# Kernel tuning notes

Measured on AMD Instinct MI355X. Metric: run time of the kernel, lower is better.

## Reference

```python
import jax, jax.numpy as jnp
import numpy as np

N = 50000
E = 800000
H = 256
ED = 13
EPS = 1e-5


def silu(x):
    return x * jax.nn.sigmoid(x)


def layernorm(x, g, b):
    mu = jnp.mean(x, axis=-1, keepdims=True)
    var = jnp.var(x, axis=-1, keepdims=True)
    return (x - mu) * jax.lax.rsqrt(var + EPS) * g + b


def setup_inputs() -> dict:
    key = jax.random.key(0)
    ks = jax.random.split(key, 24)
    s = 0.02
    d = {
        "h": jax.random.normal(ks[0], (N, H), jnp.float32),
        "pos": jax.random.normal(ks[1], (N, 3), jnp.float32),
        "edge_index": jax.random.randint(ks[2], (2, E), 0, N, jnp.int32),
        "edge_attr": jax.random.normal(ks[3], (E, ED), jnp.float32),
        # edge_mlp: Linear(2H+1+ED -> 2H), SiLU, LN(2H), Linear(2H -> H), SiLU
        "W_e1": jax.random.normal(ks[4], (2 * H + 1 + ED, 2 * H), jnp.float32) * s,
        "b_e1": jnp.zeros((2 * H,), jnp.float32),
        "g_e": jnp.ones((2 * H,), jnp.float32),
        "be_ln": jnp.zeros((2 * H,), jnp.float32),
        "W_e2": jax.random.normal(ks[5], (2 * H, H), jnp.float32) * s,
        "b_e2": jnp.zeros((H,), jnp.float32),
        # node_mlp: Linear(2H -> 2H), SiLU, LN(2H), Linear(2H -> H)
        "W_n1": jax.random.normal(ks[6], (2 * H, 2 * H), jnp.float32) * s,
        "b_n1": jnp.zeros((2 * H,), jnp.float32),
        "g_n": jnp.ones((2 * H,), jnp.float32),
        "bn_ln": jnp.zeros((2 * H,), jnp.float32),
        "W_n2": jax.random.normal(ks[7], (2 * H, H), jnp.float32) * s,
        "b_n2": jnp.zeros((H,), jnp.float32),
        # outer LayerNorm(H)
        "g_o": jnp.ones((H,), jnp.float32),
        "bo_ln": jnp.zeros((H,), jnp.float32),
        # coord_mlp: Linear(H->H), SiLU, Linear(H->1, no bias, weight*0.001)
        "W_c1": jax.random.normal(ks[8], (H, H), jnp.float32) * s,
        "b_c1": jnp.zeros((H,), jnp.float32),
        "W_c2": jax.random.normal(ks[9], (H, 1), jnp.float32) * 0.001,
        # att_mlp: Linear(H->1), Sigmoid
        "W_a": jax.random.normal(ks[10], (H, 1), jnp.float32) * s,
        "b_a": jnp.zeros((1,), jnp.float32),
        # coord_feedback: Linear(1->H), SiLU, Linear(H->H)
        "W_f1": jax.random.normal(ks[11], (1, H), jnp.float32) * s,
        "b_f1": jnp.zeros((H,), jnp.float32),
        "W_f2": jax.random.normal(ks[12], (H, H), jnp.float32) * s,
        "b_f2": jnp.zeros((H,), jnp.float32),
    }
    return d


def reference(h, pos, edge_index, edge_attr,
              W_e1, b_e1, g_e, be_ln, W_e2, b_e2,
              W_n1, b_n1, g_n, bn_ln, W_n2, b_n2,
              g_o, bo_ln,
              W_c1, b_c1, W_c2,
              W_a, b_a,
              W_f1, b_f1, W_f2, b_f2):
    row, col = edge_index[0], edge_index[1]
    diff = pos[row] - pos[col]                                  # [E,3]
    dist = jnp.maximum(jnp.linalg.norm(diff, axis=-1, keepdims=True), 1e-5)
    edge_in = jnp.concatenate([h[row], h[col], dist, edge_attr], axis=-1)
    m = silu(layernorm(silu(edge_in @ W_e1 + b_e1), g_e, be_ln) @ W_e2 + b_e2)  # [E,H]
    att = jax.nn.sigmoid(m @ W_a + b_a)                         # [E,1]
    agg = jax.ops.segment_sum(m * att, row, num_segments=N)     # [N,H]
    node_in = jnp.concatenate([h, agg], axis=-1)
    h_upd = layernorm(silu(node_in @ W_n1 + b_n1), g_n, bn_ln) @ W_n2 + b_n2
    h_new = layernorm(h + h_upd, g_o, bo_ln)
    coord_w = silu(m @ W_c1 + b_c1) @ W_c2                      # [E,1]
    coord_agg = jax.ops.segment_sum(diff * coord_w, row, num_segments=N)
    pos_new = pos + coord_agg
    diff_new = pos_new[row] - pos_new[col]
    dist_new = jnp.maximum(jnp.linalg.norm(diff_new, axis=-1, keepdims=True), 1e-5)
    coord_fb = silu(dist_new @ W_f1 + b_f1) @ W_f2 + b_f2       # [E,H]
    fb_agg = jax.ops.segment_sum(coord_fb, row, num_segments=N)
    h_new = h_new + 0.1 * fb_agg
    return (h_new, pos_new)
```

## Files before the change

kernel.cpp:

```cpp
#include <hip/hip_runtime.h>


#define NN 50000
#define EE 800000

typedef unsigned short u16;
typedef float f32x4 __attribute__((ext_vector_type(4)));
typedef short bf16x8 __attribute__((ext_vector_type(8)));
typedef unsigned uint4v __attribute__((ext_vector_type(4)));

__device__ __forceinline__ u16 f2bf(float f) {
  unsigned u = __float_as_uint(f);
  u = (u + 0x7FFFu + ((u >> 16) & 1u)) >> 16;
  return (u16)u;
}
__device__ __forceinline__ float bf2f(u16 s) {
  return __uint_as_float(((unsigned)s) << 16);
}
__device__ __forceinline__ float bflo(unsigned u) { return __uint_as_float(u << 16); }
__device__ __forceinline__ float bfhi(unsigned u) { return __uint_as_float(u & 0xFFFF0000u); }
__device__ __forceinline__ float silu_f(float x) {
  return x * __builtin_amdgcn_rcpf(1.f + exp2f(x * -1.44269504f));
}

__device__ __forceinline__ void gload16(const void* g, void* l) {
  __builtin_amdgcn_global_load_lds(
      (const __attribute__((address_space(1))) void*)g,
      (__attribute__((address_space(3))) void*)l, 16, 0, 0);
}

__global__ __launch_bounds__(256, 2) void edge_fused(
    const u16* __restrict__ P1, const u16* __restrict__ P2,
    const float* __restrict__ dist, const float* __restrict__ eattr,
    const float* __restrict__ Wt, const float* __restrict__ ge,
    const float* __restrict__ beln, const float* __restrict__ be2,
    const float* __restrict__ bc1, const float* __restrict__ Wa,
    const float* __restrict__ ba, const float* __restrict__ Wc2,
    const u16* __restrict__ We2f, const u16* __restrict__ Wc1f,
    const int* __restrict__ rowp, const int* __restrict__ colp,
    const int* __restrict__ perm, const int* __restrict__ meta, int cidx,
    u16* __restrict__ mBuf, float* __restrict__ att, float* __restrict__ cwv) {
  const int M = meta[2 * cidx + 1];
  const int eb = meta[2 * cidx];
  const int m0 = blockIdx.x * 64;
  if (m0 >= M) return;
  __shared__ __align__(16) u16 At[64][512];
  const int tid = threadIdx.x, w = tid >> 6, lane = tid & 63;
  const int l15 = lane & 15, kq = lane >> 4;
  const int ch0 = lane * 8;

  {
    int le0 = m0 + w * 16 + (lane & 15);
    if (le0 > M - 1) le0 = M - 1;
    const int e_l = perm[eb + le0];
    const int r_l = rowp[e_l];
    const int c_l = colp[e_l];
    const float dd_l = dist[e_l];

    float wreg[8][15], gg[8], bb[8];
#pragma unroll
    for (int i = 0; i < 8; i++) {
#pragma unroll
      for (int j = 0; j < 15; j++) wreg[i][j] = Wt[(ch0 + i) * 16 + j];
      gg[i] = ge[ch0 + i]; bb[i] = beln[ch0 + i];
    }
#pragma unroll 2
    for (int rr = 0; rr < 16; rr++) {
      int e = __shfl(e_l, rr);
      int r = __shfl(r_l, rr);
      int c = __shfl(c_l, rr);
      float dd = __shfl(dd_l, rr);
      float fa[13];
#pragma unroll
      for (int j = 0; j < 13; j++) fa[j] = eattr[(size_t)e * 13 + j];
      uint4v u1 = *(const uint4v*)&P1[(size_t)r * 512 + ch0];
      uint4v u2 = *(const uint4v*)&P2[(size_t)c * 512 + ch0];
      float sv[8], s1 = 0.f, s2 = 0.f;
#pragma unroll
      for (int i = 0; i < 8; i++) {
        float xp = (i & 1) ? bfhi(u1[i >> 1]) : bflo(u1[i >> 1]);
        float xq = (i & 1) ? bfhi(u2[i >> 1]) : bflo(u2[i >> 1]);
        float x = xp + xq + wreg[i][0] + dd * wreg[i][1];
#pragma unroll
        for (int j = 0; j < 13; j++) x = fmaf(fa[j], wreg[i][2 + j], x);
        float s = silu_f(x);
        sv[i] = s; s1 += s; s2 += s * s;
      }
#pragma unroll
      for (int o = 32; o; o >>= 1) { s1 += __shfl_xor(s1, o); s2 += __shfl_xor(s2, o); }
      float mu = s1 * (1.f / 512.f);
      float inv = rsqrtf(s2 * (1.f / 512.f) - mu * mu + 1e-5f);
      int row = w * 16 + rr;
      u16 ot[8];
#pragma unroll
      for (int i = 0; i < 8; i++) ot[i] = f2bf((sv[i] - mu) * inv * gg[i] + bb[i]);
      *(uint4v*)&At[row][(lane ^ (row & 7)) * 8] = *(const uint4v*)ot;
    }
  }
  __syncthreads();

  f32x4 acc[4][4] = {};
  {
    const u16* Bw = We2f + (size_t)w * 32768;
    __builtin_amdgcn_s_setprio(1);
#pragma unroll 4
    for (int ks = 0; ks < 16; ks++) {
      bf16x8 bfr[4], af[4];
#pragma unroll
      for (int j = 0; j < 4; j++)
        bfr[j] = *(const bf16x8*)&Bw[((ks * 4 + j) * 64 + lane) * 8];
#pragma unroll
      for (int i = 0; i < 4; i++) {
        int rw = i * 16 + l15;
        af[i] = *(const bf16x8*)&At[rw][((ks * 4 + kq) ^ (rw & 7)) * 8];
      }
#pragma unroll
      for (int i = 0; i < 4; i++)
#pragma unroll
        for (int j = 0; j < 4; j++)
          acc[i][j] = __builtin_amdgcn_mfma_f32_16x16x32_bf16(af[i], bfr[j], acc[i][j], 0, 0, 0);
    }
    __builtin_amdgcn_s_setprio(0);
  }
  __syncthreads();

  u16* Mt = &At[0][0];
  float* red = (float*)&At[32][0];
  float ds_a[4][4];
#pragma unroll
  for (int i = 0; i < 4; i++)
#pragma unroll
    for (int t = 0; t < 4; t++) ds_a[i][t] = 0.f;
#pragma unroll
  for (int j = 0; j < 4; j++) {
    int col = w * 64 + j * 16 + l15;
    float bz = be2[col], wa = Wa[col];
    int slot = col >> 3, offc = col & 7;
#pragma unroll
    for (int i = 0; i < 4; i++) {
#pragma unroll
      for (int t = 0; t < 4; t++) {
        int row = i * 16 + kq * 4 + t;
        float sv = silu_f(acc[i][j][t] + bz);
        int le = m0 + row;
        if (le < M) mBuf[(size_t)le * 256 + col] = f2bf(sv);
        Mt[row * 256 + ((slot ^ (row & 7)) << 3) + offc] = f2bf(sv);
        ds_a[i][t] += sv * wa;
      }
    }
  }
#pragma unroll
  for (int i = 0; i < 4; i++)
#pragma unroll
    for (int t = 0; t < 4; t++) {
      float s = ds_a[i][t];
      s += __shfl_xor(s, 1); s += __shfl_xor(s, 2);
      s += __shfl_xor(s, 4); s += __shfl_xor(s, 8);
      if (l15 == 0) red[(i * 16 + kq * 4 + t) * 4 + w] = s;
    }
  __syncthreads();
  if (tid < 64) {
    int le = m0 + tid;
    if (le < M) {
      float s = red[tid * 4] + red[tid * 4 + 1] + red[tid * 4 + 2] + red[tid * 4 + 3] + ba[0];
      att[le] = __builtin_amdgcn_rcpf(1.f + exp2f(s * -1.44269504f));
    }
  }

  f32x4 ac2[4][4] = {};
  {
    const u16* Bw = Wc1f + (size_t)w * 16384;
    __builtin_amdgcn_s_setprio(1);
#pragma unroll 4
    for (int ks = 0; ks < 8; ks++) {
      bf16x8 bfr[4], af[4];
#pragma unroll
      for (int j = 0; j < 4; j++)
        bfr[j] = *(const bf16x8*)&Bw[((ks * 4 + j) * 64 + lane) * 8];
#pragma unroll
      for (int i = 0; i < 4; i++) {
        int rw = i * 16 + l15;
        af[i] = *(const bf16x8*)&Mt[rw * 256 + (((ks * 4 + kq) ^ (rw & 7)) << 3)];
      }
#pragma unroll
      for (int i = 0; i < 4; i++)
#pragma unroll
        for (int j = 0; j < 4; j++)
          ac2[i][j] = __builtin_amdgcn_mfma_f32_16x16x32_bf16(af[i], bfr[j], ac2[i][j], 0, 0, 0);
    }
    __builtin_amdgcn_s_setprio(0);
  }
  float ds_c[4][4];
#pragma unroll
  for (int i = 0; i < 4; i++)
#pragma unroll
    for (int t = 0; t < 4; t++) ds_c[i][t] = 0.f;
#pragma unroll
  for (int j = 0; j < 4; j++) {
    int col = w * 64 + j * 16 + l15;
    float bz = bc1[col], wc = Wc2[col];
#pragma unroll
    for (int i = 0; i < 4; i++)
#pragma unroll
      for (int t = 0; t < 4; t++)
        ds_c[i][t] += silu_f(ac2[i][j][t] + bz) * wc;
  }
  __syncthreads();
#pragma unroll
  for (int i = 0; i < 4; i++)
#pragma unroll
    for (int t = 0; t < 4; t++) {
      float s = ds_c[i][t];
      s += __shfl_xor(s, 1); s += __shfl_xor(s, 2);
      s += __shfl_xor(s, 4); s += __shfl_xor(s, 8);
      if (l15 == 0) red[(i * 16 + kq * 4 + t) * 4 + w] = s;
    }
  __syncthreads();
  if (tid < 64) {
    int le = m0 + tid;
    if (le < M)
      cwv[le] = red[tid * 4] + red[tid * 4 + 1] + red[tid * 4 + 2] + red[tid * 4 + 3];
  }
}

template <int MODE, int GATHER>
__global__ __launch_bounds__(256) void gemm128(
    const u16* __restrict__ A, const u16* __restrict__ BT,
    const float* __restrict__ bias, void* __restrict__ outp,
    int Mh, int Nc, int K,
    const u16* __restrict__ hbf, const u16* __restrict__ src2,
    const float* __restrict__ cnt, const float* __restrict__ b2, float scale) {
  const int M = Mh;
  const int m0 = blockIdx.x * 128, n0 = blockIdx.y * 128;
  if (m0 >= M) return;
  __shared__ __align__(16) u16 As[128][32];
  __shared__ __align__(16) u16 Bs[128][32];
  const int tid = threadIdx.x, w = tid >> 6, lane = tid & 63;
  const int srow = lane >> 2, sch = (lane & 3) * 8;
  const int r0 = w * 32 + srow, r1 = r0 + 16;

  u16* as0 = &As[w * 32][0];
  u16* as1 = &As[w * 32 + 16][0];
  u16* bs0 = &Bs[w * 32][0];
  u16* bs1 = &Bs[w * 32 + 16][0];

  const u16 *a0r, *a0c, *a1r, *a1c;
  a0c = a1c = nullptr;
  if (GATHER == 2) {
    int q0 = m0 + r0; if (q0 > M - 1) q0 = M - 1;
    int q1 = m0 + r1; if (q1 > M - 1) q1 = M - 1;
    a0r = hbf + (size_t)q0 * 256;  a0c = src2 + (size_t)q0 * 256;
    a1r = hbf + (size_t)q1 * 256;  a1c = src2 + (size_t)q1 * 256;
  } else {
    a0r = A + (size_t)(m0 + r0) * K;
    a1r = A + (size_t)(m0 + r1) * K;
  }
  const u16* b0 = BT + (size_t)(n0 + r0) * K;
  const u16* b1 = BT + (size_t)(n0 + r1) * K;

  f32x4 acc[4][4] = {};
  const int l15 = lane & 15, ko = (lane >> 4) * 8;
  const int ar0 = (w >> 1) * 64, br0 = (w & 1) * 64;

  for (int k0 = 0; k0 < K; k0 += 32) {
    const u16 *pa0, *pa1;
    if (GATHER == 2) {
      if (k0 < 256) { pa0 = a0r + k0;         pa1 = a1r + k0; }
      else          { pa0 = a0c + (k0 - 256); pa1 = a1c + (k0 - 256); }
    } else { pa0 = a0r + k0; pa1 = a1r + k0; }
    gload16(pa0 + sch, as0);
    gload16(pa1 + sch, as1);
    gload16(b0 + k0 + sch, bs0);
    gload16(b1 + k0 + sch, bs1);
    __syncthreads();
    bf16x8 af[4], bfr[4];
#pragma unroll
    for (int i = 0; i < 4; i++)
      af[i] = *reinterpret_cast<const bf16x8*>(&As[ar0 + i * 16 + l15][ko]);
#pragma unroll
    for (int j = 0; j < 4; j++)
      bfr[j] = *reinterpret_cast<const bf16x8*>(&Bs[br0 + j * 16 + l15][ko]);
#pragma unroll
    for (int i = 0; i < 4; i++)
#pragma unroll
      for (int j = 0; j < 4; j++)
        acc[i][j] = __builtin_amdgcn_mfma_f32_16x16x32_bf16(af[i], bfr[j], acc[i][j], 0, 0, 0);
    __syncthreads();
  }

  const int rb = m0 + ar0 + ((lane >> 4) << 2);
#pragma unroll
  for (int j = 0; j < 4; j++) {
    const int gc = n0 + br0 + j * 16 + l15;
    const float bz = (MODE == 2 || MODE == 7) ? 0.f : bias[gc];
#pragma unroll
    for (int i = 0; i < 4; i++) {
#pragma unroll
      for (int t = 0; t < 4; t++) {
        const int gr = rb + i * 16 + t;
        if (gr >= M) continue;
        float v = acc[i][j][t] + bz;
        size_t oi = (size_t)gr * Nc + gc;
        if (MODE == 0)      ((u16*)outp)[oi] = f2bf(silu_f(v));
        else if (MODE == 1) ((float*)outp)[oi] = v;
        else if (MODE == 2) ((float*)outp)[oi] += scale * (v + cnt[gr] * b2[gc]);
        else if (MODE == 7) ((u16*)outp)[oi] = f2bf(v);
      }
    }
  }
}

__global__ void wtrans(const float* __restrict__ src, u16* __restrict__ dst,
                       int K, int Nn, int Kpad) {
  int t = blockIdx.x * 256 + threadIdx.x;
  if (t >= Nn * Kpad) return;
  int n = t / Kpad, k = t - n * Kpad;
  float v = (k < K) ? src[(size_t)k * Nn + n] : 0.f;
  dst[t] = f2bf(v);
}

__global__ void build_wf(const float* __restrict__ src, u16* __restrict__ dst,
                         int K, int Nn) {
  int t = blockIdx.x * 256 + threadIdx.x;
  if (t >= Nn * K) return;
  int i = t & 7;
  int lane = (t >> 3) & 63;
  int rest = t >> 9;
  int j = rest & 3;
  int rest2 = rest >> 2;
  int KS = K >> 5;
  int wv = rest2 / KS, ks = rest2 - wv * KS;
  int n = wv * 64 + j * 16 + (lane & 15);
  int k = ks * 32 + (lane >> 4) * 8 + i;
  dst[t] = f2bf(src[(size_t)k * Nn + n]);
}

__global__ void build_wt(const float* __restrict__ W_e1, const float* __restrict__ b_e1,
                         float* __restrict__ Wt) {
  int t = blockIdx.x * 256 + threadIdx.x;
  if (t >= 512 * 16) return;
  int n = t >> 4, j = t & 15;
  float v = 0.f;
  if (j == 0) v = b_e1[n];
  else if (j < 15) v = W_e1[(size_t)(511 + j) * 512 + n];
  Wt[t] = v;
}

__global__ void edge_geom(const float* __restrict__ pos, const int* __restrict__ row,
                          const int* __restrict__ colx, float* __restrict__ dist,
                          int* __restrict__ icnt) {
  int e = blockIdx.x * 256 + threadIdx.x;
  if (e >= EE) return;
  int r = row[e], c = colx[e];
  float d0 = pos[r * 3 + 0] - pos[c * 3 + 0];
  float d1 = pos[r * 3 + 1] - pos[c * 3 + 1];
  float d2 = pos[r * 3 + 2] - pos[c * 3 + 2];
  dist[e] = fmaxf(sqrtf(d0 * d0 + d1 * d1 + d2 * d2), 1e-5f);
  atomicAdd(&icnt[r], 1);
}

__global__ __launch_bounds__(1024) void scan_ptr(const int* __restrict__ icnt,
                                                 int* __restrict__ ptr) {
  __shared__ int ls[1024];
  const int t = threadIdx.x;
  const int SEG = (NN + 1023) / 1024;
  int s0 = t * SEG;
  int s1 = s0 + SEG; if (s1 > NN) s1 = NN;
  int sum = 0;
  for (int i = s0; i < s1; i++) sum += icnt[i];
  ls[t] = sum;
  __syncthreads();
  for (int off = 1; off < 1024; off <<= 1) {
    int v = (t >= off) ? ls[t - off] : 0;
    __syncthreads();
    ls[t] += v;
    __syncthreads();
  }
  int run = ls[t] - sum;
  for (int i = s0; i < s1; i++) { ptr[i] = run; run += icnt[i]; }
  if (t == 1023) ptr[NN] = ls[1023];
}

__global__ void copy_head(const int* __restrict__ ptr, int* __restrict__ head,
                          float* __restrict__ cntf) {
  int n = blockIdx.x * 256 + threadIdx.x;
  if (n >= NN) return;
  head[n] = ptr[n];
  cntf[n] = (float)(ptr[n + 1] - ptr[n]);
}

__global__ void fill_perm(const int* __restrict__ row, int* __restrict__ head,
                          int* __restrict__ perm) {
  int e = blockIdx.x * 256 + threadIdx.x;
  if (e >= EE) return;
  int p = atomicAdd(&head[row[e]], 1);
  perm[p] = e;
}

__global__ void chunk_meta(const int* __restrict__ ptr, int* __restrict__ meta,
                           int CN, int nch, int capE) {
  int c = blockIdx.x * 256 + threadIdx.x;
  if (c >= nch) return;
  int lo = c * CN;
  int hi = lo + CN; if (hi > NN) hi = NN;
  int b = ptr[lo];
  int cc = ptr[hi] - b;
  if (cc > capE) cc = capE;
  meta[2 * c + 0] = b;
  meta[2 * c + 1] = cc;
}

__global__ __launch_bounds__(128) void ln_512(u16* __restrict__ t,
                                              const float* __restrict__ g,
                                              const float* __restrict__ b, int Mh) {
  int row = blockIdx.x;
  if (row >= Mh) return;
  int tid = threadIdx.x;
  size_t base = (size_t)row * 512 + tid * 4;
  ushort4 xv = *reinterpret_cast<const ushort4*>(&t[base]);
  float x0 = bf2f(xv.x), x1 = bf2f(xv.y), x2 = bf2f(xv.z), x3 = bf2f(xv.w);
  float s1 = x0 + x1 + x2 + x3;
  float s2 = x0 * x0 + x1 * x1 + x2 * x2 + x3 * x3;
  for (int o = 32; o; o >>= 1) { s1 += __shfl_xor(s1, o); s2 += __shfl_xor(s2, o); }
  __shared__ float red[4];
  if ((tid & 63) == 0) { red[tid >> 6] = s1; red[2 + (tid >> 6)] = s2; }
  __syncthreads();
  s1 = red[0] + red[1]; s2 = red[2] + red[3];
  float mu = s1 * (1.f / 512.f);
  float var = s2 * (1.f / 512.f) - mu * mu;
  float inv = rsqrtf(var + 1e-5f);
  int c = tid * 4;
  ushort4 yv;
  yv.x = f2bf((x0 - mu) * inv * g[c + 0] + b[c + 0]);
  yv.y = f2bf((x1 - mu) * inv * g[c + 1] + b[c + 1]);
  yv.z = f2bf((x2 - mu) * inv * g[c + 2] + b[c + 2]);
  yv.w = f2bf((x3 - mu) * inv * g[c + 3] + b[c + 3]);
  *reinterpret_cast<ushort4*>(&t[base]) = yv;
}

__global__ __launch_bounds__(256) void node_agg(
    const u16* __restrict__ m, const float* __restrict__ att,
    const float* __restrict__ cwv,
    const float* __restrict__ pos, const int* __restrict__ colx,
    const int* __restrict__ perm, const int* __restrict__ ptr,
    const int* __restrict__ meta, int cidx,
    u16* __restrict__ aggbf, float* __restrict__ cagg, int nlo, int cn) {
  int w = threadIdx.x >> 6, lane = threadIdx.x & 63;
  int nl = blockIdx.x * 4 + w;
  if (nl >= cn) return;
  int n = nlo + nl;
  int base = meta[2 * cidx];
  int p0 = ptr[n], p1 = ptr[n + 1];
  const int half = lane >> 5, ch = (lane & 31) * 8;
  float a[8] = {};
  for (int p = p0 + half; p < p1; p += 2) {
    int le = p - base;
    float at = att[le];
    uint4v mv = *reinterpret_cast<const uint4v*>(&m[(size_t)le * 256 + ch]);
#pragma unroll
    for (int i = 0; i < 4; i++) {
      a[2 * i]     += at * bflo(mv[i]);
      a[2 * i + 1] += at * bfhi(mv[i]);
    }
  }
#pragma unroll
  for (int i = 0; i < 8; i++) a[i] += __shfl_xor(a[i], 32);
  if (half == 0) {
    u16 ot[8];
#pragma unroll
    for (int i = 0; i < 8; i++) ot[i] = f2bf(a[i]);
    *reinterpret_cast<uint4v*>(&aggbf[(size_t)n * 256 + ch]) =
        *reinterpret_cast<const uint4v*>(ot);
  }
  float prx = pos[n * 3 + 0], pry = pos[n * 3 + 1], prz = pos[n * 3 + 2];
  float sx = 0.f, sy = 0.f, sz = 0.f;
  for (int p = p0 + lane; p < p1; p += 64) {
    int le = p - base;
    float cv = cwv[le];
    int c = colx[perm[p]];
    sx += cv * (prx - pos[c * 3 + 0]);
    sy += cv * (pry - pos[c * 3 + 1]);
    sz += cv * (prz - pos[c * 3 + 2]);
  }
#pragma unroll
  for (int o = 32; o; o >>= 1) {
    sx += __shfl_xor(sx, o); sy += __shfl_xor(sy, o); sz += __shfl_xor(sz, o);
  }
  if (lane == 0) {
    cagg[n * 3 + 0] = sx; cagg[n * 3 + 1] = sy; cagg[n * 3 + 2] = sz;
  }
}

__global__ __launch_bounds__(64) void hmid_ln(const float* __restrict__ h,
                                              const float* __restrict__ hupd,
                                              const float* __restrict__ g,
                                              const float* __restrict__ b,
                                              float* __restrict__ outp) {
  int row = blockIdx.x, lane = threadIdx.x;
  size_t base = (size_t)row * 256 + lane * 4;
  float x[4];
#pragma unroll
  for (int i = 0; i < 4; i++) x[i] = h[base + i] + hupd[base + i];
  float s1 = x[0] + x[1] + x[2] + x[3];
  float s2 = x[0] * x[0] + x[1] * x[1] + x[2] * x[2] + x[3] * x[3];
  for (int o = 32; o; o >>= 1) { s1 += __shfl_xor(s1, o); s2 += __shfl_xor(s2, o); }
  float mu = s1 * (1.f / 256.f);
  float var = s2 * (1.f / 256.f) - mu * mu;
  float inv = rsqrtf(var + 1e-5f);
#pragma unroll
  for (int i = 0; i < 4; i++)
    outp[base + i] = (x[i] - mu) * inv * g[lane * 4 + i] + b[lane * 4 + i];
}

__global__ void posnew_k(const float* __restrict__ pos, const float* __restrict__ cagg,
                         float* __restrict__ op) {
  int t = blockIdx.x * 256 + threadIdx.x;
  if (t >= NN * 3) return;
  op[t] = pos[t] + cagg[t];
}

__global__ void dnn_k(const float* __restrict__ posn, const int* __restrict__ rowp,
                      const int* __restrict__ colp, const int* __restrict__ perm,
                      float* __restrict__ dnc) {
  int p = blockIdx.x * 256 + threadIdx.x;
  if (p >= EE) return;
  int e = perm[p];
  int r = rowp[e], c = colp[e];
  float d0 = posn[r * 3 + 0] - posn[c * 3 + 0];
  float d1 = posn[r * 3 + 1] - posn[c * 3 + 1];
  float d2 = posn[r * 3 + 2] - posn[c * 3 + 2];
  dnc[p] = fmaxf(sqrtf(d0 * d0 + d1 * d1 + d2 * d2), 1e-5f);
}

__global__ __launch_bounds__(256) void edge_fb2(
    const float* __restrict__ dnc, const int* __restrict__ ptr,
    const float* __restrict__ Wf1, const float* __restrict__ bf1,
    u16* __restrict__ Sbf) {
  int w = threadIdx.x >> 6, lane = threadIdx.x & 63;
  int n = blockIdx.x * 4 + w;
  if (n >= NN) return;
  const float L2E = 1.44269504f;
  float w0 = Wf1[lane * 4 + 0], w1 = Wf1[lane * 4 + 1];
  float w2 = Wf1[lane * 4 + 2], w3 = Wf1[lane * 4 + 3];
  float b0 = bf1[lane * 4 + 0], b1 = bf1[lane * 4 + 1];
  float b2 = bf1[lane * 4 + 2], b3 = bf1[lane * 4 + 3];
  float wl0 = -w0 * L2E, wl1 = -w1 * L2E, wl2 = -w2 * L2E, wl3 = -w3 * L2E;
  float bl0 = -b0 * L2E, bl1 = -b1 * L2E, bl2 = -b2 * L2E, bl3 = -b3 * L2E;
  float a0 = 0.f, a1 = 0.f, a2 = 0.f, a3 = 0.f;
  int p0 = ptr[n], p1 = ptr[n + 1];
  for (int p = p0; p < p1; p++) {
    float dn = dnc[p];
    float x0 = fmaf(dn, w0, b0), e0 = exp2f(fmaf(dn, wl0, bl0));
    float x1 = fmaf(dn, w1, b1), e1 = exp2f(fmaf(dn, wl1, bl1));
    float x2 = fmaf(dn, w2, b2), e2 = exp2f(fmaf(dn, wl2, bl2));
    float x3 = fmaf(dn, w3, b3), e3 = exp2f(fmaf(dn, wl3, bl3));
    a0 += x0 * __builtin_amdgcn_rcpf(1.f + e0);
    a1 += x1 * __builtin_amdgcn_rcpf(1.f + e1);
    a2 += x2 * __builtin_amdgcn_rcpf(1.f + e2);
    a3 += x3 * __builtin_amdgcn_rcpf(1.f + e3);
  }
  ushort4 ov;
  ov.x = f2bf(a0); ov.y = f2bf(a1); ov.z = f2bf(a2); ov.w = f2bf(a3);
  *reinterpret_cast<ushort4*>(&Sbf[(size_t)n * 256 + lane * 4]) = ov;
}

__global__ void cvt_bf(const float* __restrict__ src, u16* __restrict__ dst, int n) {
  int t = blockIdx.x * 256 + threadIdx.x;
  if (t < n) dst[t] = f2bf(src[t]);
}

extern "C" void kernel_launch(void* const* d_in, const int* in_sizes, int n_in,
                              void* d_out, int out_size, void* d_ws, size_t ws_size,
                              hipStream_t stream) {
  const float* h     = (const float*)d_in[0];
  const float* pos   = (const float*)d_in[1];
  const int*   eidx  = (const int*)d_in[2];
  const float* eattr = (const float*)d_in[3];
  const float* W_e1 = (const float*)d_in[4];  const float* b_e1 = (const float*)d_in[5];
  const float* g_e  = (const float*)d_in[6];  const float* be_ln = (const float*)d_in[7];
  const float* W_e2 = (const float*)d_in[8];  const float* b_e2 = (const float*)d_in[9];
  const float* W_n1 = (const float*)d_in[10]; const float* b_n1 = (const float*)d_in[11];
  const float* g_n  = (const float*)d_in[12]; const float* bn_ln = (const float*)d_in[13];
  const float* W_n2 = (const float*)d_in[14]; const float* b_n2 = (const float*)d_in[15];
  const float* g_o  = (const float*)d_in[16]; const float* bo_ln = (const float*)d_in[17];
  const float* W_c1 = (const float*)d_in[18]; const float* b_c1 = (const float*)d_in[19];
  const float* W_c2 = (const float*)d_in[20];
  const float* W_a  = (const float*)d_in[21]; const float* b_a = (const float*)d_in[22];
  const float* W_f1 = (const float*)d_in[23]; const float* b_f1 = (const float*)d_in[24];
  const float* W_f2 = (const float*)d_in[25]; const float* b_f2 = (const float*)d_in[26];

  float* outp = (float*)d_out;
  float* out_pos = outp + (size_t)NN * 256;

  char* base = (char*)d_ws;
  size_t off = 0;
  auto alloc = [&](size_t bytes) -> void* {
    off = (off + 255) & ~(size_t)255;
    void* p = base + off;
    off += bytes;
    return p;
  };
  const int NP = 50048;
  u16* We1Ta = (u16*)alloc((size_t)512 * 256 * 2);
  u16* We1Tb = (u16*)alloc((size_t)512 * 256 * 2);
  u16* We2f  = (u16*)alloc((size_t)256 * 512 * 2);
  u16* Wc1f  = (u16*)alloc((size_t)256 * 256 * 2);
  u16* Wn1T  = (u16*)alloc((size_t)512 * 512 * 2);
  u16* Wn2T  = (u16*)alloc((size_t)256 * 512 * 2);
  u16* Wf2T  = (u16*)alloc((size_t)256 * 256 * 2);
  float* Wt  = (float*)alloc((size_t)512 * 16 * 4);
  u16* hbf   = (u16*)alloc((size_t)NP * 256 * 2);
  float* dist = (float*)alloc((size_t)EE * 4);
  int*   icnt = (int*)alloc((size_t)NN * 4);
  int*   ptr  = (int*)alloc((size_t)(NN + 1) * 4);
  int*   head = (int*)alloc((size_t)NN * 4);
  int*   perm = (int*)alloc((size_t)EE * 4);
  float* cntf = (float*)alloc((size_t)NN * 4);
  float* cagg = (float*)alloc((size_t)NN * 12);
  int*   meta = (int*)alloc((size_t)8192);
  u16*   aggbf = (u16*)alloc((size_t)NP * 256 * 2);
  u16*   P1 = (u16*)alloc((size_t)NP * 512 * 2);
  u16*   P2 = (u16*)alloc((size_t)NP * 512 * 2);

  off = (off + 255) & ~(size_t)255;
  char* arena = base + off;
  size_t avail = (ws_size > off) ? ws_size - off : 0;
  const size_t SBF_BYTES = (size_t)NP * 256 * 2;
  const int ladder[6] = {16384, 12288, 8192, 4096, 2048, 1024};
  int CN = 1024;
  for (int li = 0; li < 6; li++) {
    size_t need = (size_t)((size_t)ladder[li] * 16 + 4096) * 520;
    if (need < SBF_BYTES) need = SBF_BYTES;
    if (need <= avail) { CN = ladder[li]; break; }
  }
  const int capE = CN * 16 + 4096;
  u16*   mBuf = (u16*)arena;
  float* att  = (float*)(arena + (size_t)capE * 512);
  float* cw   = (float*)(arena + (size_t)capE * 516);
  u16*   Sbf  = (u16*)arena;
  u16*   t2   = P1;
  float* hupd = (float*)P2;

  const int* rowp = eidx;
  const int* colp = eidx + EE;
  const int nch = (NN + CN - 1) / CN;

  hipMemsetAsync(icnt, 0, (size_t)NN * 4, stream);

  wtrans<<<(512 * 256 + 255) / 256, 256, 0, stream>>>(W_e1, We1Ta, 256, 512, 256);
  wtrans<<<(512 * 256 + 255) / 256, 256, 0, stream>>>(W_e1 + (size_t)256 * 512, We1Tb, 256, 512, 256);
  build_wf<<<(256 * 512 + 255) / 256, 256, 0, stream>>>(W_e2, We2f, 512, 256);
  build_wf<<<(256 * 256 + 255) / 256, 256, 0, stream>>>(W_c1, Wc1f, 256, 256);
  wtrans<<<(512 * 512 + 255) / 256, 256, 0, stream>>>(W_n1, Wn1T, 512, 512, 512);
  wtrans<<<(256 * 512 + 255) / 256, 256, 0, stream>>>(W_n2, Wn2T, 512, 256, 512);
  wtrans<<<(256 * 256 + 255) / 256, 256, 0, stream>>>(W_f2, Wf2T, 256, 256, 256);
  build_wt<<<(512 * 16 + 255) / 256, 256, 0, stream>>>(W_e1, b_e1, Wt);
  cvt_bf<<<(NN * 256 + 255) / 256, 256, 0, stream>>>(h, hbf, NN * 256);

  edge_geom<<<(EE + 255) / 256, 256, 0, stream>>>(pos, rowp, colp, dist, icnt);
  scan_ptr<<<1, 1024, 0, stream>>>(icnt, ptr);
  copy_head<<<(NN + 255) / 256, 256, 0, stream>>>(ptr, head, cntf);
  fill_perm<<<(EE + 255) / 256, 256, 0, stream>>>(rowp, head, perm);
  chunk_meta<<<(nch + 255) / 256, 256, 0, stream>>>(ptr, meta, CN, nch, capE);

  dim3 gp(NP / 128, 4);
  gemm128<7, 0><<<gp, 256, 0, stream>>>(hbf, We1Ta, nullptr, P1, NN, 512, 256,
                                        nullptr, nullptr, nullptr, nullptr, 0.f);
  gemm128<7, 0><<<gp, 256, 0, stream>>>(hbf, We1Tb, nullptr, P2, NN, 512, 256,
                                        nullptr, nullptr, nullptr, nullptr, 0.f);

  for (int c = 0; c < nch; c++) {
    int nlo = c * CN;
    int cn = NN - nlo; if (cn > CN) cn = CN;
    edge_fused<<<capE / 64, 256, 0, stream>>>(
        P1, P2, dist, eattr, Wt, g_e, be_ln, b_e2, b_c1, W_a, b_a, W_c2,
        We2f, Wc1f, rowp, colp, perm, meta, c, mBuf, att, cw);
    node_agg<<<(cn + 3) / 4, 256, 0, stream>>>(mBuf, att, cw, pos, colp, perm, ptr,
                                               meta, c, aggbf, cagg, nlo, cn);
  }

  gemm128<0, 2><<<gp, 256, 0, stream>>>(nullptr, Wn1T, b_n1, t2, NN, 512, 512,
                                        hbf, aggbf, nullptr, nullptr, 0.f);
  ln_512<<<NN, 128, 0, stream>>>(t2, g_n, bn_ln, NN);
  dim3 g5(NP / 128, 2);
  gemm128<1, 0><<<g5, 256, 0, stream>>>(t2, Wn2T, b_n2, hupd, NN, 256, 512,
                                        nullptr, nullptr, nullptr, nullptr, 0.f);
  hmid_ln<<<NN, 64, 0, stream>>>(h, hupd, g_o, bo_ln, outp);

  posnew_k<<<(NN * 3 + 255) / 256, 256, 0, stream>>>(pos, cagg, out_pos);
  dnn_k<<<(EE + 255) / 256, 256, 0, stream>>>(out_pos, rowp, colp, perm, dist);
  edge_fb2<<<(NN + 3) / 4, 256, 0, stream>>>(dist, ptr, W_f1, b_f1, Sbf);
  gemm128<2, 0><<<g5, 256, 0, stream>>>(Sbf, Wf2T, nullptr, outp, NN, 256, 256,
                                        nullptr, nullptr, cntf, b_f2, 0.1f);
}
```

Baseline: 1.941 ms.

## Compute first edge-MLP layer per edge with MFMA instead of node-level projections

Replaces the precomputed node-level projections P1/P2 (h@W_e1 halves, gathered per edge) with a per-edge MFMA GEMM over the full 527-wide edge input. The kernel gathers h rows by row/col index and reads a per-chunk bf16 tail buffer holding bias, distance and edge attributes, built by a new small kernel. The LayerNorm reduction now goes through shared memory across waves. This trades two node GEMMs and their 512-wide gathers for about 16x more first-layer FLOPs on edges. It also enlarges the chunk-size ladder and adds a kernel launch per chunk.

```diff
diff --git a/kernel.cpp b/kernel.cpp
--- a/kernel.cpp
+++ b/kernel.cpp
@@ -30,13 +30,13 @@
 }
 
 __global__ __launch_bounds__(256, 2) void edge_fused(
-    const u16* __restrict__ P1, const u16* __restrict__ P2,
-    const float* __restrict__ dist, const float* __restrict__ eattr,
-    const float* __restrict__ Wt, const float* __restrict__ ge,
-    const float* __restrict__ beln, const float* __restrict__ be2,
-    const float* __restrict__ bc1, const float* __restrict__ Wa,
-    const float* __restrict__ ba, const float* __restrict__ Wc2,
-    const u16* __restrict__ We2f, const u16* __restrict__ Wc1f,
+    const u16* __restrict__ hbf, const u16* __restrict__ tail,
+    const float* __restrict__ ge, const float* __restrict__ beln,
+    const float* __restrict__ be2, const float* __restrict__ bc1,
+    const float* __restrict__ Wa, const float* __restrict__ ba,
+    const float* __restrict__ Wc2,
+    const u16* __restrict__ We1f, const u16* __restrict__ We2f,
+    const u16* __restrict__ Wc1f,
     const int* __restrict__ rowp, const int* __restrict__ colp,
     const int* __restrict__ perm, const int* __restrict__ meta, int cidx,
     u16* __restrict__ mBuf, float* __restrict__ att, float* __restrict__ cwv) {
@@ -47,55 +47,106 @@
   __shared__ __align__(16) u16 At[64][512];
   const int tid = threadIdx.x, w = tid >> 6, lane = tid & 63;
   const int l15 = lane & 15, kq = lane >> 4;
-  const int ch0 = lane * 8;
-
+
+  int ridx[4], cidx4[4], tle[4];
+#pragma unroll
+  for (int i = 0; i < 4; i++) {
+    int le = m0 + i * 16 + l15; if (le > M - 1) le = M - 1;
+    tle[i] = le;
+    int e = perm[eb + le];
+    ridx[i] = rowp[e]; cidx4[i] = colp[e];
+  }
+  float gg[8], bb[8];
+#pragma unroll
+  for (int j = 0; j < 8; j++) {
+    int col = w * 128 + j * 16 + l15;
+    gg[j] = ge[col]; bb[j] = beln[col];
+  }
+
+  f32x4 acc1[4][8] = {};
   {
-    int le0 = m0 + w * 16 + (lane & 15);
-    if (le0 > M - 1) le0 = M - 1;
-    const int e_l = perm[eb + le0];
-    const int r_l = rowp[e_l];
-    const int c_l = colp[e_l];
-    const float dd_l = dist[e_l];
-
-    float wreg[8][15], gg[8], bb[8];
-#pragma unroll
-    for (int i = 0; i < 8; i++) {
-#pragma unroll
-      for (int j = 0; j < 15; j++) wreg[i][j] = Wt[(ch0 + i) * 16 + j];
-      gg[i] = ge[ch0 + i]; bb[i] = beln[ch0 + i];
-    }
-#pragma unroll 2
-    for (int rr = 0; rr < 16; rr++) {
-      int e = __shfl(e_l, rr);
-      int r = __shfl(r_l, rr);
-      int c = __shfl(c_l, rr);
-      float dd = __shfl(dd_l, rr);
-      float fa[13];
-#pragma unroll
-      for (int j = 0; j < 13; j++) fa[j] = eattr[(size_t)e * 13 + j];
-      uint4v u1 = *(const uint4v*)&P1[(size_t)r * 512 + ch0];
-      uint4v u2 = *(const uint4v*)&P2[(size_t)c * 512 + ch0];
-      float sv[8], s1 = 0.f, s2 = 0.f;
-#pragma unroll
-      for (int i = 0; i < 8; i++) {
-        float xp = (i & 1) ? bfhi(u1[i >> 1]) : bflo(u1[i >> 1]);
-        float xq = (i & 1) ? bfhi(u2[i >> 1]) : bflo(u2[i >> 1]);
-        float x = xp + xq + wreg[i][0] + dd * wreg[i][1];
-#pragma unroll
-        for (int j = 0; j < 13; j++) x = fmaf(fa[j], wreg[i][2 + j], x);
-        float s = silu_f(x);
-        sv[i] = s; s1 += s; s2 += s * s;
-      }
-#pragma unroll
-      for (int o = 32; o; o >>= 1) { s1 += __shfl_xor(s1, o); s2 += __shfl_xor(s2, o); }
-      float mu = s1 * (1.f / 512.f);
-      float inv = rsqrtf(s2 * (1.f / 512.f) - mu * mu + 1e-5f);
-      int row = w * 16 + rr;
-      u16 ot[8];
-#pragma unroll
-      for (int i = 0; i < 8; i++) ot[i] = f2bf((sv[i] - mu) * inv * gg[i] + bb[i]);
-      *(uint4v*)&At[row][(lane ^ (row & 7)) * 8] = *(const uint4v*)ot;
-    }
+    const u16* Bw1 = We1f + (size_t)w * 69632;
+    for (int ks = 0; ks < 17; ks++) {
+      bf16x8 af[4];
+#pragma unroll
+      for (int i = 0; i < 4; i++) {
+        const u16* ap;
+        if (ks < 8)       ap = hbf + (size_t)ridx[i] * 256 + ks * 32 + kq * 8;
+        else if (ks < 16) ap = hbf + (size_t)cidx4[i] * 256 + (ks - 8) * 32 + kq * 8;
+        else              ap = tail + (size_t)tle[i] * 32 + kq * 8;
+        af[i] = *(const bf16x8*)ap;
+      }
+      __builtin_amdgcn_s_setprio(1);
+#pragma unroll
+      for (int j = 0; j < 8; j++) {
+        bf16x8 bfr = *(const bf16x8*)&Bw1[((size_t)(ks * 8 + j) * 64 + lane) * 8];
+#pragma unroll
+        for (int i = 0; i < 4; i++)
+          acc1[i][j] = __builtin_amdgcn_mfma_f32_16x16x32_bf16(af[i], bfr, acc1[i][j], 0, 0, 0);
+      }
+      __builtin_amdgcn_s_setprio(0);
+    }
+  }
+
+  {
+    float* red2 = (float*)&At[0][0];
+    float s1a[4][4], s2a[4][4];
+#pragma unroll
+    for (int i = 0; i < 4; i++)
+#pragma unroll
+      for (int t = 0; t < 4; t++) { s1a[i][t] = 0.f; s2a[i][t] = 0.f; }
+#pragma unroll
+    for (int i = 0; i < 4; i++)
+#pragma unroll
+      for (int j = 0; j < 8; j++)
+#pragma unroll
+        for (int t = 0; t < 4; t++) {
+          float sv = silu_f(acc1[i][j][t]);
+          acc1[i][j][t] = sv;
+          s1a[i][t] += sv; s2a[i][t] += sv * sv;
+        }
+#pragma unroll
+    for (int i = 0; i < 4; i++)
+#pragma unroll
+      for (int t = 0; t < 4; t++) {
+        float s1 = s1a[i][t], s2 = s2a[i][t];
+        s1 += __shfl_xor(s1, 1); s2 += __shfl_xor(s2, 1);
+        s1 += __shfl_xor(s1, 2); s2 += __shfl_xor(s2, 2);
+        s1 += __shfl_xor(s1, 4); s2 += __shfl_xor(s2, 4);
+        s1 += __shfl_xor(s1, 8); s2 += __shfl_xor(s2, 8);
+        if (l15 == 0) {
+          int row = i * 16 + kq * 4 + t;
+          red2[row * 8 + w * 2] = s1;
+          red2[row * 8 + w * 2 + 1] = s2;
+        }
+      }
+    __syncthreads();
+    float muv[4][4], invv[4][4];
+#pragma unroll
+    for (int i = 0; i < 4; i++)
+#pragma unroll
+      for (int t = 0; t < 4; t++) {
+        int row = i * 16 + kq * 4 + t;
+        float s1 = red2[row * 8 + 0] + red2[row * 8 + 2] + red2[row * 8 + 4] + red2[row * 8 + 6];
+        float s2 = red2[row * 8 + 1] + red2[row * 8 + 3] + red2[row * 8 + 5] + red2[row * 8 + 7];
+        float mu = s1 * (1.f / 512.f);
+        muv[i][t] = mu;
+        invv[i][t] = rsqrtf(s2 * (1.f / 512.f) - mu * mu + 1e-5f);
+      }
+    __syncthreads();
+#pragma unroll
+    for (int i = 0; i < 4; i++)
+#pragma unroll
+      for (int j = 0; j < 8; j++) {
+        int col = w * 128 + j * 16 + l15;
+        int slot = col >> 3, offc = col & 7;
+#pragma unroll
+        for (int t = 0; t < 4; t++) {
+          int row = i * 16 + kq * 4 + t;
+          float val = (acc1[i][j][t] - muv[i][t]) * invv[i][t] * gg[j] + bb[j];
+          At[row][(((slot) ^ (row & 7)) << 3) | offc] = f2bf(val);
+        }
+      }
   }
   __syncthreads();
 
@@ -335,15 +386,38 @@
   dst[t] = f2bf(src[(size_t)k * Nn + n]);
 }
 
-__global__ void build_wt(const float* __restrict__ W_e1, const float* __restrict__ b_e1,
-                         float* __restrict__ Wt) {
+__global__ void build_we1f(const float* __restrict__ W_e1, const float* __restrict__ b_e1,
+                           u16* __restrict__ dst) {
   int t = blockIdx.x * 256 + threadIdx.x;
-  if (t >= 512 * 16) return;
-  int n = t >> 4, j = t & 15;
+  if (t >= 4 * 17 * 8 * 64 * 8) return;
+  int i = t & 7;
+  int lane = (t >> 3) & 63;
+  int j = (t >> 9) & 7;
+  int rest = t >> 12;
+  int ks = rest % 17, wv = rest / 17;
+  int n = wv * 128 + j * 16 + (lane & 15);
+  int k = ks * 32 + (lane >> 4) * 8 + i;
   float v = 0.f;
-  if (j == 0) v = b_e1[n];
-  else if (j < 15) v = W_e1[(size_t)(511 + j) * 512 + n];
-  Wt[t] = v;
+  if (k < 512) v = W_e1[(size_t)k * 512 + n];
+  else if (k == 512) v = b_e1[n];
+  else if (k == 513) v = W_e1[(size_t)512 * 512 + n];
+  else if (k <= 526) v = W_e1[(size_t)(k - 1) * 512 + n];
+  dst[t] = f2bf(v);
+}
+
+__global__ void build_tail(const float* __restrict__ dist, const float* __restrict__ eattr,
+                           const int* __restrict__ perm, const int* __restrict__ meta,
+                           int cidx, u16* __restrict__ tail, int capE) {
+  int t = blockIdx.x * 256 + threadIdx.x;
+  if (t >= capE * 32) return;
+  int le = t >> 5, j = t & 31;
+  if (le >= meta[2 * cidx + 1]) return;
+  int e = perm[meta[2 * cidx] + le];
+  float v = 0.f;
+  if (j == 0) v = 1.f;
+  else if (j == 1) v = dist[e];
+  else if (j < 15) v = eattr[(size_t)e * 13 + (j - 2)];
+  tail[t] = f2bf(v);
 }
 
 __global__ void edge_geom(const float* __restrict__ pos, const int* __restrict__ row,
@@ -601,14 +675,12 @@
     return p;
   };
   const int NP = 50048;
-  u16* We1Ta = (u16*)alloc((size_t)512 * 256 * 2);
-  u16* We1Tb = (u16*)alloc((size_t)512 * 256 * 2);
+  u16* We1f  = (u16*)alloc((size_t)4 * 17 * 8 * 64 * 8 * 2);
   u16* We2f  = (u16*)alloc((size_t)256 * 512 * 2);
   u16* Wc1f  = (u16*)alloc((size_t)256 * 256 * 2);
   u16* Wn1T  = (u16*)alloc((size_t)512 * 512 * 2);
   u16* Wn2T  = (u16*)alloc((size_t)256 * 512 * 2);
   u16* Wf2T  = (u16*)alloc((size_t)256 * 256 * 2);
-  float* Wt  = (float*)alloc((size_t)512 * 16 * 4);
   u16* hbf   = (u16*)alloc((size_t)NP * 256 * 2);
   float* dist = (float*)alloc((size_t)EE * 4);
   int*   icnt = (int*)alloc((size_t)NN * 4);
@@ -619,27 +691,26 @@
   float* cagg = (float*)alloc((size_t)NN * 12);
   int*   meta = (int*)alloc((size_t)8192);
   u16*   aggbf = (u16*)alloc((size_t)NP * 256 * 2);
-  u16*   P1 = (u16*)alloc((size_t)NP * 512 * 2);
-  u16*   P2 = (u16*)alloc((size_t)NP * 512 * 2);
+  u16*   t2   = (u16*)alloc((size_t)NP * 512 * 2);
+  float* hupd = (float*)alloc((size_t)NP * 256 * 4);
 
   off = (off + 255) & ~(size_t)255;
   char* arena = base + off;
   size_t avail = (ws_size > off) ? ws_size - off : 0;
   const size_t SBF_BYTES = (size_t)NP * 256 * 2;
-  const int ladder[6] = {16384, 12288, 8192, 4096, 2048, 1024};
-  int CN = 1024;
-  for (int li = 0; li < 6; li++) {
-    size_t need = (size_t)((size_t)ladder[li] * 16 + 4096) * 520;
+  const int ladder[7] = {49152, 32768, 24576, 16384, 12288, 8192, 4096};
+  int CN = 4096;
+  for (int li = 0; li < 7; li++) {
+    size_t need = (size_t)((size_t)ladder[li] * 16 + 4096) * 584;
     if (need < SBF_BYTES) need = SBF_BYTES;
     if (need <= avail) { CN = ladder[li]; break; }
   }
   const int capE = CN * 16 + 4096;
   u16*   mBuf = (u16*)arena;
-  float* att  = (float*)(arena + (size_t)capE * 512);
-  float* cw   = (float*)(arena + (size_t)capE * 516);
+  u16*   tail = (u16*)(arena + (size_t)capE * 512);
+  float* att  = (float*)(arena + (size_t)capE * 576);
+  float* cw   = (float*)(arena + (size_t)capE * 580);
   u16*   Sbf  = (u16*)arena;
-  u16*   t2   = P1;
-  float* hupd = (float*)P2;
 
   const int* rowp = eidx;
   const int* colp = eidx + EE;
@@ -647,14 +718,12 @@
 
   hipMemsetAsync(icnt, 0, (size_t)NN * 4, stream);
 
-  wtrans<<<(512 * 256 + 255) / 256, 256, 0, stream>>>(W_e1, We1Ta, 256, 512, 256);
-  wtrans<<<(512 * 256 + 255) / 256, 256, 0, stream>>>(W_e1 + (size_t)256 * 512, We1Tb, 256, 512, 256);
+  build_we1f<<<(4 * 17 * 8 * 64 * 8 + 255) / 256, 256, 0, stream>>>(W_e1, b_e1, We1f);
   build_wf<<<(256 * 512 + 255) / 256, 256, 0, stream>>>(W_e2, We2f, 512, 256);
   build_wf<<<(256 * 256 + 255) / 256, 256, 0, stream>>>(W_c1, Wc1f, 256, 256);
   wtrans<<<(512 * 512 + 255) / 256, 256, 0, stream>>>(W_n1, Wn1T, 512, 512, 512);
   wtrans<<<(256 * 512 + 255) / 256, 256, 0, stream>>>(W_n2, Wn2T, 512, 256, 512);
   wtrans<<<(256 * 256 + 255) / 256, 256, 0, stream>>>(W_f2, Wf2T, 256, 256, 256);
-  build_wt<<<(512 * 16 + 255) / 256, 256, 0, stream>>>(W_e1, b_e1, Wt);
   cvt_bf<<<(NN * 256 + 255) / 256, 256, 0, stream>>>(h, hbf, NN * 256);
 
   edge_geom<<<(EE + 255) / 256, 256, 0, stream>>>(pos, rowp, colp, dist, icnt);
@@ -663,22 +732,18 @@
   fill_perm<<<(EE + 255) / 256, 256, 0, stream>>>(rowp, head, perm);
   chunk_meta<<<(nch + 255) / 256, 256, 0, stream>>>(ptr, meta, CN, nch, capE);
 
-  dim3 gp(NP / 128, 4);
-  gemm128<7, 0><<<gp, 256, 0, stream>>>(hbf, We1Ta, nullptr, P1, NN, 512, 256,
-                                        nullptr, nullptr, nullptr, nullptr, 0.f);
-  gemm128<7, 0><<<gp, 256, 0, stream>>>(hbf, We1Tb, nullptr, P2, NN, 512, 256,
-                                        nullptr, nullptr, nullptr, nullptr, 0.f);
-
   for (int c = 0; c < nch; c++) {
     int nlo = c * CN;
     int cn = NN - nlo; if (cn > CN) cn = CN;
+    build_tail<<<(capE * 32 + 255) / 256, 256, 0, stream>>>(dist, eattr, perm, meta, c, tail, capE);
     edge_fused<<<capE / 64, 256, 0, stream>>>(
-        P1, P2, dist, eattr, Wt, g_e, be_ln, b_e2, b_c1, W_a, b_a, W_c2,
-        We2f, Wc1f, rowp, colp, perm, meta, c, mBuf, att, cw);
+        hbf, tail, g_e, be_ln, b_e2, b_c1, W_a, b_a, W_c2,
+        We1f, We2f, Wc1f, rowp, colp, perm, meta, c, mBuf, att, cw);
     node_agg<<<(cn + 3) / 4, 256, 0, stream>>>(mBuf, att, cw, pos, colp, perm, ptr,
                                                meta, c, aggbf, cagg, nlo, cn);
   }
 
+  dim3 gp(NP / 128, 4);
   gemm128<0, 2><<<gp, 256, 0, stream>>>(nullptr, Wn1T, b_n1, t2, NN, 512, 512,
                                         hbf, aggbf, nullptr, nullptr, 0.f);
   ln_512<<<NN, 128, 0, stream>>>(t2, g_n, bn_ln, NN);
```

After: 2.570 ms. +32.4%, slower.

## Process edges within each chunk in column-sorted order for gather locality

Applied to the files above, without the earlier changes.

Adds a per-chunk counting sort of edges by destination column (histogram, scan, scatter) that produces a secondary permutation. The fused edge kernel walks edges in this column-sorted order, so gathers of P2 rows for the same column land close together and reuse cache. Outputs are still written to their original slot positions, so node aggregation is unchanged. The cost is three extra kernels, a memset sized chunks × N, and scattered writes to mBuf, att and cw.

```diff
diff --git a/kernel.cpp b/kernel.cpp
--- a/kernel.cpp
+++ b/kernel.cpp
@@ -38,20 +38,27 @@
     const float* __restrict__ ba, const float* __restrict__ Wc2,
     const u16* __restrict__ We2f, const u16* __restrict__ Wc1f,
     const int* __restrict__ rowp, const int* __restrict__ colp,
-    const int* __restrict__ perm, const int* __restrict__ meta, int cidx,
+    const int* __restrict__ perm, const int* __restrict__ sperm,
+    const int* __restrict__ meta, int cidx,
     u16* __restrict__ mBuf, float* __restrict__ att, float* __restrict__ cwv) {
   const int M = meta[2 * cidx + 1];
   const int eb = meta[2 * cidx];
   const int m0 = blockIdx.x * 64;
   if (m0 >= M) return;
   __shared__ __align__(16) u16 At[64][512];
+  __shared__ int sle[64];
   const int tid = threadIdx.x, w = tid >> 6, lane = tid & 63;
   const int l15 = lane & 15, kq = lane >> 4;
   const int ch0 = lane * 8;
 
+  if (tid < 64) {
+    int sq = m0 + tid; if (sq > M - 1) sq = M - 1;
+    sle[tid] = sperm[eb + sq];
+  }
+  __syncthreads();
+
   {
-    int le0 = m0 + w * 16 + (lane & 15);
-    if (le0 > M - 1) le0 = M - 1;
+    const int le0 = sle[w * 16 + (lane & 15)];
     const int e_l = perm[eb + le0];
     const int r_l = rowp[e_l];
     const int c_l = colp[e_l];
@@ -142,8 +149,8 @@
       for (int t = 0; t < 4; t++) {
         int row = i * 16 + kq * 4 + t;
         float sv = silu_f(acc[i][j][t] + bz);
-        int le = m0 + row;
-        if (le < M) mBuf[(size_t)le * 256 + col] = f2bf(sv);
+        if (m0 + row < M)
+          mBuf[(size_t)sle[row] * 256 + col] = f2bf(sv);
         Mt[row * 256 + ((slot ^ (row & 7)) << 3) + offc] = f2bf(sv);
         ds_a[i][t] += sv * wa;
       }
@@ -160,10 +167,9 @@
     }
   __syncthreads();
   if (tid < 64) {
-    int le = m0 + tid;
-    if (le < M) {
+    if (m0 + tid < M) {
       float s = red[tid * 4] + red[tid * 4 + 1] + red[tid * 4 + 2] + red[tid * 4 + 3] + ba[0];
-      att[le] = __builtin_amdgcn_rcpf(1.f + exp2f(s * -1.44269504f));
+      att[sle[tid]] = __builtin_amdgcn_rcpf(1.f + exp2f(s * -1.44269504f));
     }
   }
 
@@ -217,9 +223,8 @@
     }
   __syncthreads();
   if (tid < 64) {
-    int le = m0 + tid;
-    if (le < M)
-      cwv[le] = red[tid * 4] + red[tid * 4 + 1] + red[tid * 4 + 2] + red[tid * 4 + 3];
+    if (m0 + tid < M)
+      cwv[sle[tid]] = red[tid * 4] + red[tid * 4 + 1] + red[tid * 4 + 2] + red[tid * 4 + 3];
   }
 }
 
@@ -408,6 +413,49 @@
   if (cc > capE) cc = capE;
   meta[2 * c + 0] = b;
   meta[2 * c + 1] = cc;
+}
+
+__global__ void chist(const int* __restrict__ colp, const int* __restrict__ perm,
+                      const int* __restrict__ meta, int nch, int* __restrict__ hist) {
+  int p = blockIdx.x * 256 + threadIdx.x;
+  if (p >= EE) return;
+  int c = nch - 1;
+  while (c > 0 && p < meta[2 * c]) c--;
+  atomicAdd(&hist[(size_t)c * NN + colp[perm[p]]], 1);
+}
+
+__global__ __launch_bounds__(1024) void cscan(int* __restrict__ data) {
+  int c = blockIdx.x;
+  int* d = data + (size_t)c * NN;
+  __shared__ int ls[1024];
+  const int t = threadIdx.x;
+  const int SEG = (NN + 1023) / 1024;
+  int s0 = t * SEG;
+  int s1 = s0 + SEG; if (s1 > NN) s1 = NN;
+  int sum = 0;
+  for (int i = s0; i < s1; i++) sum += d[i];
+  ls[t] = sum;
+  __syncthreads();
+  for (int off = 1; off < 1024; off <<= 1) {
+    int v = (t >= off) ? ls[t - off] : 0;
+    __syncthreads();
+    ls[t] += v;
+    __syncthreads();
+  }
+  int run = ls[t] - sum;
+  for (int i = s0; i < s1; i++) { int cc = d[i]; d[i] = run; run += cc; }
+}
+
+__global__ void cscatter(const int* __restrict__ colp, const int* __restrict__ perm,
+                         const int* __restrict__ meta, int nch,
+                         int* __restrict__ chead, int* __restrict__ sperm) {
+  int p = blockIdx.x * 256 + threadIdx.x;
+  if (p >= EE) return;
+  int c = nch - 1;
+  while (c > 0 && p < meta[2 * c]) c--;
+  int b = meta[2 * c];
+  int q = atomicAdd(&chead[(size_t)c * NN + colp[perm[p]]], 1);
+  sperm[b + q] = p - b;
 }
 
 __global__ __launch_bounds__(128) void ln_512(u16* __restrict__ t,
@@ -615,6 +663,7 @@
   int*   ptr  = (int*)alloc((size_t)(NN + 1) * 4);
   int*   head = (int*)alloc((size_t)NN * 4);
   int*   perm = (int*)alloc((size_t)EE * 4);
+  int*   sperm = (int*)alloc((size_t)EE * 4);
   float* cntf = (float*)alloc((size_t)NN * 4);
   float* cagg = (float*)alloc((size_t)NN * 12);
   int*   meta = (int*)alloc((size_t)8192);
@@ -629,23 +678,27 @@
   const int ladder[6] = {16384, 12288, 8192, 4096, 2048, 1024};
   int CN = 1024;
   for (int li = 0; li < 6; li++) {
-    size_t need = (size_t)((size_t)ladder[li] * 16 + 4096) * 520;
+    int nchl = (NN + ladder[li] - 1) / ladder[li];
+    size_t need = (size_t)((size_t)ladder[li] * 16 + 4096) * 520 +
+                  (size_t)nchl * NN * 4 + 512;
     if (need < SBF_BYTES) need = SBF_BYTES;
     if (need <= avail) { CN = ladder[li]; break; }
   }
   const int capE = CN * 16 + 4096;
+  const int nch = (NN + CN - 1) / CN;
   u16*   mBuf = (u16*)arena;
   float* att  = (float*)(arena + (size_t)capE * 512);
   float* cw   = (float*)(arena + (size_t)capE * 516);
+  int*   csort = (int*)(arena + (((size_t)capE * 520 + 255) & ~(size_t)255));
   u16*   Sbf  = (u16*)arena;
   u16*   t2   = P1;
   float* hupd = (float*)P2;
 
   const int* rowp = eidx;
   const int* colp = eidx + EE;
-  const int nch = (NN + CN - 1) / CN;
 
   hipMemsetAsync(icnt, 0, (size_t)NN * 4, stream);
+  hipMemsetAsync(csort, 0, (size_t)nch * NN * 4, stream);
 
   wtrans<<<(512 * 256 + 255) / 256, 256, 0, stream>>>(W_e1, We1Ta, 256, 512, 256);
   wtrans<<<(512 * 256 + 255) / 256, 256, 0, stream>>>(W_e1 + (size_t)256 * 512, We1Tb, 256, 512, 256);
@@ -662,6 +715,9 @@
   copy_head<<<(NN + 255) / 256, 256, 0, stream>>>(ptr, head, cntf);
   fill_perm<<<(EE + 255) / 256, 256, 0, stream>>>(rowp, head, perm);
   chunk_meta<<<(nch + 255) / 256, 256, 0, stream>>>(ptr, meta, CN, nch, capE);
+  chist<<<(EE + 255) / 256, 256, 0, stream>>>(colp, perm, meta, nch, csort);
+  cscan<<<nch, 1024, 0, stream>>>(csort);
+  cscatter<<<(EE + 255) / 256, 256, 0, stream>>>(colp, perm, meta, nch, csort, sperm);
 
   dim3 gp(NP / 128, 4);
   gemm128<7, 0><<<gp, 256, 0, stream>>>(hbf, We1Ta, nullptr, P1, NN, 512, 256,
@@ -674,7 +730,7 @@
     int cn = NN - nlo; if (cn > CN) cn = CN;
     edge_fused<<<capE / 64, 256, 0, stream>>>(
         P1, P2, dist, eattr, Wt, g_e, be_ln, b_e2, b_c1, W_a, b_a, W_c2,
-        We2f, Wc1f, rowp, colp, perm, meta, c, mBuf, att, cw);
+        We2f, Wc1f, rowp, colp, perm, sperm, meta, c, mBuf, att, cw);
     node_agg<<<(cn + 3) / 4, 256, 0, stream>>>(mBuf, att, cw, pos, colp, perm, ptr,
                                                meta, c, aggbf, cagg, nlo, cn);
   }
```

After: 2.208 ms. 1.14x slower.
